# Kernel tuning notes

Measured on AMD Instinct MI355X. Metric: run time of the kernel, lower is better.

Reference implementation:

```python
import jax, jax.numpy as jnp
import numpy as np
import math

DIM = 1024
NUM_HEADS = 16
HEAD_DIM = DIM // NUM_HEADS
EPS = 1e-6
DILATED = 2
WINDOW = 2  # window_size init arg; actual window = L * WINDOW per side


def setup_inputs() -> dict:
    key = jax.random.key(0)
    ks = jax.random.split(key, 14)
    B, S = 1, 8704
    x = jax.random.normal(ks[0], (B, S, DIM), jnp.float32)
    ang = jax.random.uniform(ks[1], (S, HEAD_DIM // 2), jnp.float32, -jnp.pi, jnp.pi)
    freqs_cos = jnp.cos(ang)
    freqs_sin = jnp.sin(ang)
    def lin(k):
        return 0.02 * jax.random.normal(k, (DIM, DIM), jnp.float32)
    def bias(k):
        return 0.01 * jax.random.normal(k, (DIM,), jnp.float32)
    return {
        'x': x, 'freqs_cos': freqs_cos, 'freqs_sin': freqs_sin,
        'wq': lin(ks[2]), 'bq': bias(ks[3]),
        'wk': lin(ks[4]), 'bk': bias(ks[5]),
        'wv': lin(ks[6]), 'bv': bias(ks[7]),
        'wo': lin(ks[8]), 'bo': bias(ks[9]),
        'gq': 1.0 + 0.02 * jax.random.normal(ks[10], (DIM,), jnp.float32),
        'gk': 1.0 + 0.02 * jax.random.normal(ks[11], (DIM,), jnp.float32),
        'f': 34, 'L': 256,
    }


def rmsnorm(h, g):
    return h * jax.lax.rsqrt(jnp.mean(h * h, axis=-1, keepdims=True) + EPS) * g


def rope(h, cos, sin):
    # h: [B,S,D] viewed as interleaved complex pairs per head, rotated by unit freqs
    B, S, D = h.shape
    hp = h.reshape(B, S, NUM_HEADS, HEAD_DIM // 2, 2)
    a, b = hp[..., 0], hp[..., 1]
    c = cos[None, :, None, :]
    s = sin[None, :, None, :]
    ra = a * c - b * s
    rb = a * s + b * c
    return jnp.stack([ra, rb], axis=-1).reshape(B, S, D)


def windowed_attention(q, k, v, w):
    # sliding-window attention: query i attends keys j with |i-j| <= w (inclusive)
    B, S, D = q.shape
    H, hd = NUM_HEADS, HEAD_DIM
    def heads(t):
        return t.reshape(B, S, H, hd).transpose(0, 2, 1, 3)  # [B,H,S,hd]
    qh, kh, vh = heads(q), heads(k), heads(v)
    C = w  # block size == window -> only 3 neighbor key blocks per query block
    pad = (-S) % C
    Sp = S + pad
    nb = Sp // C
    def blocks(t):
        return jnp.pad(t, ((0, 0), (0, 0), (0, pad), (0, 0))).reshape(B, H, nb, C, hd)
    qb = blocks(qh)
    def win(t):
        tb = jnp.pad(blocks(t), ((0, 0), (0, 0), (1, 1), (0, 0), (0, 0)))
        return jnp.concatenate([tb[:, :, i:i + nb] for i in range(3)], axis=3)  # [B,H,nb,3C,hd]
    kw_, vw_ = win(kh), win(vh)
    scores = jnp.einsum('bhnqd,bhnkd->bhnqk', qb, kw_) * (1.0 / math.sqrt(hd))
    qi = jnp.arange(nb)[:, None, None] * C + jnp.arange(C)[None, :, None]      # [nb,C,1]
    kj = (jnp.arange(nb)[:, None, None] - 1) * C + jnp.arange(3 * C)[None, None, :]  # [nb,1,3C]
    valid = (kj >= 0) & (kj < S) & (qi - kj <= w) & (kj - qi <= w)
    scores = jnp.where(valid, scores, -1e9)
    p = jax.nn.softmax(scores, axis=-1)
    o = jnp.einsum('bhnqk,bhnkd->bhnqd', p, vw_)
    return o.reshape(B, H, Sp, hd)[:, :, :S].transpose(0, 2, 1, 3).reshape(B, S, D)


def reference(x, freqs_cos, freqs_sin, wq, bq, wk, bk, wv, bv, wo, bo, gq, gk, f, L):
    B, S, D = x.shape
    q = rope(rmsnorm(x @ wq + bq, gq), freqs_cos, freqs_sin)
    k = rope(rmsnorm(x @ wk + bk, gk), freqs_cos, freqs_sin)
    v = x @ wv + bv
    w = L * WINDOW
    use_dilated = DILATED > 1 and S // (DILATED * L) > 1
    if use_dilated:
        blk = DILATED * L
        pad_len = blk - S % blk  # == blk when S % blk == 0 (faithful to torch code)
        Sp = S + pad_len
        n = Sp // blk
        def padd(t):
            return jnp.pad(t, ((0, 0), (0, pad_len), (0, 0)))
        def dil(t):
            # 'b (n d l) c -> (b d) (n l) c'
            return t.reshape(B, n, DILATED, L, D).transpose(0, 2, 1, 3, 4).reshape(B * DILATED, n * L, D)
        q, k, v = dil(padd(q)), dil(padd(k)), dil(padd(v))
    o = windowed_attention(q, k, v, w)
    out = o @ wo + bo
    if use_dilated:
        # '(b d) (n l) c -> b (n d l) c', then drop pad
        out = out.reshape(B, DILATED, n, L, D).transpose(0, 2, 1, 3, 4).reshape(B, n * DILATED * L, D)
        out = out[:, :S]
    return out
```

## Files before the change

### kernel.cpp

```cpp
#include <hip/hip_runtime.h>
#include <hip/hip_bf16.h>
#include <stdint.h>

#define DIM 1024
#define NH 16
#define HD 64
#define S_ORIG 8704
#define WIN 512

typedef __attribute__((ext_vector_type(8))) short short8;
typedef __attribute__((ext_vector_type(4))) float f32x4;
typedef __attribute__((ext_vector_type(16))) float f32x16;

__device__ __forceinline__ float bf2f(unsigned short u) {
    return __uint_as_float(((unsigned int)u) << 16);
}
__device__ __forceinline__ unsigned short f2bf(float f) {
    unsigned int x = __float_as_uint(f);
    unsigned int r = x + 0x7fffu + ((x >> 16) & 1u);
    return (unsigned short)(r >> 16);
}
__device__ __forceinline__ unsigned int cvtpk(float lo, float hi) {
    unsigned int r;
    asm("v_cvt_pk_bf16_f32 %0, %1, %2" : "=v"(r) : "v"(lo), "v"(hi));
    return r;
}
__device__ __forceinline__ float fexp2(float x) {
#if __has_builtin(__builtin_amdgcn_exp2f)
    return __builtin_amdgcn_exp2f(x);
#else
    float r;
    asm("v_exp_f32 %0, %1" : "=v"(r) : "v"(x));
    return r;
#endif
}

#define GLD_LDS(gptr, lptr) \
    __builtin_amdgcn_global_load_lds((const __attribute__((address_space(1))) void*)(gptr), \
                                     (__attribute__((address_space(3))) void*)(lptr), 16, 0, 0)

#define FBAR() do { __asm__ volatile("" ::: "memory"); \
                    __builtin_amdgcn_s_barrier(); \
                    __asm__ volatile("" ::: "memory"); } while (0)

__global__ __launch_bounds__(256) void prep(const float* __restrict__ x,
                                            unsigned short* __restrict__ xb,
                                            const float* __restrict__ w0,
                                            const float* __restrict__ w1,
                                            const float* __restrict__ w2,
                                            const float* __restrict__ w3,
                                            unsigned short* __restrict__ wt) {
    __shared__ float ts[64][65];
    const int bx = blockIdx.x;
    const int t = threadIdx.x;
    if (bx < 8704) {
        int i = (bx * 256 + t) * 4;
        float4 v = *(const float4*)(x + i);
        ushort4 o;
        o.x = f2bf(v.x); o.y = f2bf(v.y); o.z = f2bf(v.z); o.w = f2bf(v.w);
        *(ushort4*)(xb + i) = o;
        return;
    }
    const int b = bx - 8704;
    const int z = b >> 8;
    const int rem = b & 255;
    const int kb = (rem >> 4) * 64, nb = (rem & 15) * 64;
    const float* w = z == 0 ? w0 : z == 1 ? w1 : z == 2 ? w2 : w3;
    unsigned short* o = wt + (size_t)z * DIM * DIM;
    const int c = t & 63, r4 = t >> 6;
#pragma unroll
    for (int rr = 0; rr < 16; rr++) {
        int row = rr * 4 + r4;
        ts[row][c] = w[(size_t)(kb + row) * DIM + nb + c];
    }
    __syncthreads();
#pragma unroll
    for (int rr = 0; rr < 16; rr++) {
        int nl = rr * 4 + r4;
        o[(size_t)(nb + nl) * DIM + kb + c] = f2bf(ts[c][nl]);
    }
}

__device__ __forceinline__ void gemm_step(const unsigned short* __restrict__ pa,
                                          const unsigned short* __restrict__ pb,
                                          int wr, int wc, int r, int jsw,
                                          f32x4 acc[4][4]) {
    short8 af[4], bfr[4];
#pragma unroll
    for (int i = 0; i < 4; i++)
        af[i] = *(const short8*)&pa[(wr * 64 + i * 16 + r) * 32 + jsw];
#pragma unroll
    for (int j = 0; j < 4; j++)
        bfr[j] = *(const short8*)&pb[(wc * 64 + j * 16 + r) * 32 + jsw];
#pragma unroll
    for (int i = 0; i < 4; i++)
#pragma unroll
        for (int j = 0; j < 4; j++)
            acc[i][j] = __builtin_amdgcn_mfma_f32_16x16x32_bf16(af[i], bfr[j], acc[i][j], 0, 0, 0);
}

template <int OUTF32>
__global__ __launch_bounds__(256) void gemm_bf16(const unsigned short* __restrict__ A,
                                                 const unsigned short* __restrict__ Bt,
                                                 const float* __restrict__ b0,
                                                 const float* __restrict__ b1,
                                                 const float* __restrict__ b2,
                                                 void* __restrict__ Cout) {
    __shared__ __align__(16) unsigned short As[3][128 * 32];
    __shared__ __align__(16) unsigned short Bs[3][128 * 32];
    const int z = blockIdx.z;
    const unsigned short* B = Bt + (size_t)z * DIM * DIM;
    const float* bias = z == 0 ? b0 : (z == 1 ? b1 : b2);
    const int m0 = blockIdx.x * 128, n0 = blockIdx.y * 128;
    const int tid = threadIdx.x;
    const int lane = tid & 63, wv = tid >> 6;
    const int wr = wv >> 1, wc = wv & 1;
    const int quad = lane >> 4, r = lane & 15;

    f32x4 acc[4][4];
#pragma unroll
    for (int i = 0; i < 4; i++)
#pragma unroll
        for (int j = 0; j < 4; j++)
#pragma unroll
            for (int t4 = 0; t4 < 4; t4++) acc[i][j][t4] = 0.0f;

    const unsigned short* a_base = A + (size_t)m0 * DIM;
    const unsigned short* b_base = B + (size_t)n0 * DIM;
    const int c0 = wv * 128 + lane;
    const int r0 = c0 >> 2, o0 = (((c0 & 3) ^ ((c0 >> 3) & 3))) * 8;
    const int c1 = c0 + 64;
    const int r1 = c1 >> 2, o1 = (((c1 & 3) ^ ((c1 >> 3) & 3))) * 8;
    const int ld0 = (wv * 128) * 8, ld1 = (wv * 128 + 64) * 8;

    const int jsw = (quad ^ ((r >> 1) & 3)) * 8;

#define ISSUE_STEP(k0_, abuf_, bbuf_) do {                                  \
        GLD_LDS(a_base + (size_t)r0 * DIM + (k0_) + o0, (abuf_) + ld0);     \
        GLD_LDS(a_base + (size_t)r1 * DIM + (k0_) + o1, (abuf_) + ld1);     \
        GLD_LDS(b_base + (size_t)r0 * DIM + (k0_) + o0, (bbuf_) + ld0);     \
        GLD_LDS(b_base + (size_t)r1 * DIM + (k0_) + o1, (bbuf_) + ld1);     \
    } while (0)

    unsigned short *pa0 = &As[0][0], *pa1 = &As[1][0], *pa2 = &As[2][0];
    unsigned short *pb0 = &Bs[0][0], *pb1 = &Bs[1][0], *pb2 = &Bs[2][0];

    ISSUE_STEP(0, pa0, pb0);
    ISSUE_STEP(32, pa1, pb1);

#pragma unroll 3
    for (int k0 = 0; k0 < DIM - 64; k0 += 32) {
        FBAR();
        ISSUE_STEP(k0 + 64, pa2, pb2);
        __asm__ volatile("s_waitcnt vmcnt(8)" ::: "memory");
        __builtin_amdgcn_sched_barrier(0);
        FBAR();
        gemm_step(pa0, pb0, wr, wc, r, jsw, acc);
        unsigned short* t;
        t = pa0; pa0 = pa1; pa1 = pa2; pa2 = t;
        t = pb0; pb0 = pb1; pb1 = pb2; pb2 = t;
    }
    __asm__ volatile("s_waitcnt vmcnt(4)" ::: "memory");
    __builtin_amdgcn_sched_barrier(0);
    FBAR();
    gemm_step(pa0, pb0, wr, wc, r, jsw, acc);
    {
        unsigned short* t;
        t = pa0; pa0 = pa1; pa1 = pa2; pa2 = t;
        t = pb0; pb0 = pb1; pb1 = pb2; pb2 = t;
    }
    __asm__ volatile("s_waitcnt vmcnt(0)" ::: "memory");
    __builtin_amdgcn_sched_barrier(0);
    FBAR();
    gemm_step(pa0, pb0, wr, wc, r, jsw, acc);
#undef ISSUE_STEP

#pragma unroll
    for (int i = 0; i < 4; i++) {
        const int row = m0 + wr * 64 + i * 16 + quad * 4;
#pragma unroll
        for (int j = 0; j < 4; j++) {
            const int col = n0 + wc * 64 + j * 16 + r;
            const float bvl = bias[col];
#pragma unroll
            for (int t4 = 0; t4 < 4; t4++) {
                float vv = acc[i][j][t4] + bvl;
                if (OUTF32) {
                    ((float*)Cout)[(size_t)(row + t4) * DIM + col] = vv;
                } else {
                    ((unsigned short*)Cout)[(size_t)z * S_ORIG * DIM + (size_t)(row + t4) * DIM + col] = f2bf(vv);
                }
            }
        }
    }
}

__global__ __launch_bounds__(256) void norm_rope(unsigned short* __restrict__ hq,
                                                 unsigned short* __restrict__ hk,
                                                 const float* __restrict__ gq,
                                                 const float* __restrict__ gk,
                                                 const float* __restrict__ fcos,
                                                 const float* __restrict__ fsin) {
    const int z = blockIdx.y;
    unsigned short* h = z == 0 ? hq : hk;
    const float* g = z == 0 ? gq : gk;
    const int w = threadIdx.x >> 6, lane = threadIdx.x & 63;
    const int srow = blockIdx.x * 4 + w;
    unsigned short* hp = h + (size_t)srow * DIM;
    const int p0 = lane * 8, p1 = 512 + lane * 8;

    union { int4 i4; unsigned short u[8]; } r0, r1, o0, o1;
    r0.i4 = *(const int4*)(hp + p0);
    r1.i4 = *(const int4*)(hp + p1);
    float v[16];
#pragma unroll
    for (int j = 0; j < 8; j++) { v[j] = bf2f(r0.u[j]); v[8 + j] = bf2f(r1.u[j]); }

    float ss = 0.0f;
#pragma unroll
    for (int j = 0; j < 16; j++) ss += v[j] * v[j];
#pragma unroll
    for (int off = 1; off < 64; off <<= 1) ss += __shfl_xor(ss, off, 64);
    const float rinv = rsqrtf(ss * (1.0f / DIM) + 1e-6f);

    float4 ga = *(const float4*)(g + p0), gb = *(const float4*)(g + p0 + 4);
    float4 gc = *(const float4*)(g + p1), gd = *(const float4*)(g + p1 + 4);
    const float* gg[4] = {&ga.x, &gb.x, &gc.x, &gd.x};
#pragma unroll
    for (int q4 = 0; q4 < 4; q4++)
#pragma unroll
        for (int j = 0; j < 4; j++) v[q4 * 4 + j] *= rinv * gg[q4][j];

    const int i0 = (p0 & 63) >> 1;
    float4 cs = *(const float4*)(fcos + (size_t)srow * 32 + i0);
    float4 sn = *(const float4*)(fsin + (size_t)srow * 32 + i0);
    const float* cp = &cs.x;
    const float* sp = &sn.x;
#pragma unroll
    for (int seg = 0; seg < 2; seg++) {
        unsigned short* uo = seg == 0 ? o0.u : o1.u;
#pragma unroll
        for (int pr = 0; pr < 4; pr++) {
            const float a = v[seg * 8 + pr * 2], b = v[seg * 8 + pr * 2 + 1];
            uo[pr * 2]     = f2bf(a * cp[pr] - b * sp[pr]);
            uo[pr * 2 + 1] = f2bf(a * sp[pr] + b * cp[pr]);
        }
    }
    *(int4*)(hp + p0) = o0.i4;
    *(int4*)(hp + p1) = o1.i4;
}

__device__ __forceinline__ void softmax16(f32x16& s, int kk0, int hi4, int qi,
                                          bool edge, float& lsum) {
#pragma unroll
    for (int reg = 0; reg < 16; reg++) {
        float e = fexp2(s[reg]);
        if (edge) {
            const int kj = kk0 + (reg & 3) + 8 * (reg >> 2) + hi4;
            const int dl = qi - kj;
            if (dl > WIN || dl < -WIN) e = 0.0f;
        }
        s[reg] = e;
        lsum += e;
    }
}

__device__ __forceinline__ short8 mkfrag(const f32x16& p, int base) {
    unsigned int a0 = cvtpk(p[base + 0], p[base + 1]);
    unsigned int b0 = cvtpk(p[base + 4], p[base + 5]);
    unsigned int a1 = cvtpk(p[base + 2], p[base + 3]);
    unsigned int b1 = cvtpk(p[base + 6], p[base + 7]);
    asm volatile("v_permlane32_swap_b32 %0, %1" : "+v"(a0), "+v"(b0));
    asm volatile("v_permlane32_swap_b32 %0, %1" : "+v"(a1), "+v"(b1));
    union { unsigned int w[4]; short8 s; } u;
    u.w[0] = a0; u.w[1] = a1; u.w[2] = b0; u.w[3] = b1;
    return u.s;
}

__device__ __forceinline__ void pack_write_v(unsigned short* __restrict__ Vt,
                                             int4 a0i, int4 a1i, int vt_d0, int vkc, int vko) {
    union { int4 i4; unsigned int w[4]; } a0, a1;
    a0.i4 = a0i; a1.i4 = a1i;
#pragma unroll
    for (int dw = 0; dw < 4; dw++) {
        unsigned int lo = __builtin_amdgcn_perm(a1.w[dw], a0.w[dw], 0x05040100u);
        unsigned int hw = __builtin_amdgcn_perm(a1.w[dw], a0.w[dw], 0x07060302u);
        *(unsigned int*)&Vt[(vt_d0 + dw * 2) * 64 + ((vkc ^ (dw * 2)) << 3) + vko] = lo;
        *(unsigned int*)&Vt[(vt_d0 + dw * 2 + 1) * 64 + ((vkc ^ (dw * 2 + 1)) << 3) + vko] = hw;
    }
}

__global__ __launch_bounds__(256) void attn(const unsigned short* __restrict__ qkv,
                                            unsigned short* __restrict__ ob) {
    __shared__ __align__(16) unsigned short Ks[2][64 * 64];
    __shared__ __align__(16) unsigned short Vt[64 * 64];

    const int head = blockIdx.x >> 1;
    const int d = blockIdx.x & 1;
    const int t0 = blockIdx.y * 2, t1 = t0 + 1;
    const int tid = threadIdx.x;
    const int lane = tid & 63, wv = tid >> 6;
    const int hi = lane >> 5, q32 = lane & 31;
    const int sw8 = (q32 & 7);

    const unsigned short* qb = qkv;
    const unsigned short* kb = qkv + (size_t)S_ORIG * DIM;
    const unsigned short* vb = qkv + (size_t)2 * S_ORIG * DIM;

    const int tw = t0 + (wv >> 1);
    const int qi = tw * 64 + (wv & 1) * 32 + q32;
    const int og_q = ((qi >> 8) << 9) + d * 256 + (qi & 255);

    short8 qf[4];
    {
        const float QSC = 0.125f * 1.44269504088896f;
        const unsigned short* qrow = qb + (size_t)og_q * DIM + head * HD + hi * 8;
#pragma unroll
        for (int kd = 0; kd < 4; kd++) {
            union { int4 i4; unsigned short u[8]; short8 s8; } iv, ov;
            iv.i4 = *(const int4*)(qrow + kd * 16);
#pragma unroll
            for (int j = 0; j < 8; j++) ov.u[j] = f2bf(bf2f(iv.u[j]) * QSC);
            qf[kd] = ov.s8;
        }
    }

    f32x16 o0, o1;
#pragma unroll
    for (int i = 0; i < 16; i++) { o0[i] = 0.0f; o1[i] = 0.0f; }
    float lsum = 0.0f;

    const int kt_lo = (t0 - 8 > 0) ? (t0 - 8) : 0;
    const int kt_hi = (t1 + 8 < 67) ? (t1 + 8) : 67;

    const int krow0 = tid >> 3;
    const int kgc = ((tid & 7) ^ (krow0 & 7)) * 8;

    const int vt_kk = (tid & 31) * 2, vt_d0 = (tid >> 5) * 8;
    const int vkc = vt_kk >> 3, vko = vt_kk & 7;

#define ISSUE_K(kbase_, bufb_) do {                                              \
        const int kj0_ = (kbase_) + krow0;                                       \
        const int ok0_ = ((kj0_ >> 8) << 9) + d * 256 + (kj0_ & 255);            \
        GLD_LDS(kb + (size_t)ok0_ * DIM + head * HD + kgc, (bufb_) + wv * 512);  \
        const int kj1_ = kj0_ + 32;                                              \
        const int ok1_ = ((kj1_ >> 8) << 9) + d * 256 + (kj1_ & 255);            \
        GLD_LDS(kb + (size_t)ok1_ * DIM + head * HD + kgc, (bufb_) + 2048 + wv * 512); \
    } while (0)

#define LOAD_V(kbase_, a0_, a1_) do {                                            \
        const int kj_ = (kbase_) + vt_kk;                                        \
        const int ok_ = ((kj_ >> 8) << 9) + d * 256 + (kj_ & 255);               \
        (a0_) = *(const int4*)(vb + (size_t)ok_ * DIM + head * HD + vt_d0);      \
        (a1_) = *(const int4*)(vb + (size_t)(ok_ + 1) * DIM + head * HD + vt_d0);\
    } while (0)

    ISSUE_K(kt_lo * 64, &Ks[0][0]);
    int4 vc0, vc1;
    LOAD_V(kt_lo * 64, vc0, vc1);

    int cur = 0;
    for (int kt = kt_lo; kt <= kt_hi; kt++) {
        const int kbase = kt * 64;
        FBAR();

        const int knb = ((kt < kt_hi) ? (kt + 1) : kt_hi) * 64;
        ISSUE_K(knb, &Ks[cur ^ 1][0]);
        int4 vn0, vn1;
        LOAD_V(knb, vn0, vn1);

        __asm__ volatile("s_waitcnt vmcnt(4)" ::: "memory");
        __builtin_amdgcn_sched_barrier(0);

        pack_write_v(&Vt[0], vc0, vc1, vt_d0, vkc, vko);
        __asm__ volatile("s_waitcnt lgkmcnt(0)" ::: "memory");
        FBAR();

        if (kt >= tw - 8 && kt <= tw + 8) {
            const bool edge = (kt == tw - 8) || (kt == tw + 8);
            const unsigned short* K = &Ks[cur][0];

            f32x16 s0, s1;
#pragma unroll
            for (int i = 0; i < 16; i++) { s0[i] = 0.0f; s1[i] = 0.0f; }
#pragma unroll
            for (int kd = 0; kd < 4; kd++) {
                const int c = ((kd * 2 + hi) ^ sw8) << 3;
                short8 k0 = *(const short8*)&K[q32 * 64 + c];
                short8 k1 = *(const short8*)&K[(32 + q32) * 64 + c];
                s0 = __builtin_amdgcn_mfma_f32_32x32x16_bf16(k0, qf[kd], s0, 0, 0, 0);
                s1 = __builtin_amdgcn_mfma_f32_32x32x16_bf16(k1, qf[kd], s1, 0, 0, 0);
            }

            const int hi4 = hi * 4;
            softmax16(s0, kbase, hi4, qi, edge, lsum);
            softmax16(s1, kbase + 32, hi4, qi, edge, lsum);
            short8 pf0 = mkfrag(s0, 0), pf1 = mkfrag(s0, 8);
            short8 pf2 = mkfrag(s1, 0), pf3 = mkfrag(s1, 8);

#pragma unroll
            for (int kw = 0; kw < 4; kw++) {
                const int c = ((kw * 2 + hi) ^ sw8) << 3;
                short8 v0 = *(const short8*)&Vt[q32 * 64 + c];
                short8 v1 = *(const short8*)&Vt[(32 + q32) * 64 + c];
                const short8 pf = kw == 0 ? pf0 : kw == 1 ? pf1 : kw == 2 ? pf2 : pf3;
                o0 = __builtin_amdgcn_mfma_f32_32x32x16_bf16(v0, pf, o0, 0, 0, 0);
                o1 = __builtin_amdgcn_mfma_f32_32x32x16_bf16(v1, pf, o1, 0, 0, 0);
            }
        }

        vc0 = vn0; vc1 = vn1;
        cur ^= 1;
    }
#undef ISSUE_K
#undef LOAD_V

    __asm__ volatile("" :: "v"(vc0.x), "v"(vc0.y), "v"(vc0.z), "v"(vc0.w),
                          "v"(vc1.x), "v"(vc1.y), "v"(vc1.z), "v"(vc1.w));
    __asm__ volatile("s_waitcnt vmcnt(0)" ::: "memory");

    lsum += __shfl_xor(lsum, 32, 64);
    {
        const int cnt = (qi + WIN < 4607 ? qi + WIN : 4607) - 4351;
        if (cnt > 0) lsum += (float)cnt;
    }
    const float linv = 1.0f / lsum;

    unsigned short* obase = ob + (size_t)og_q * DIM + head * HD + hi * 4;
#pragma unroll
    for (int g = 0; g < 4; g++) {
        ushort4 u0, u1;
        u0.x = f2bf(o0[g * 4 + 0] * linv);
        u0.y = f2bf(o0[g * 4 + 1] * linv);
        u0.z = f2bf(o0[g * 4 + 2] * linv);
        u0.w = f2bf(o0[g * 4 + 3] * linv);
        *(ushort4*)(obase + g * 8) = u0;
        u1.x = f2bf(o1[g * 4 + 0] * linv);
        u1.y = f2bf(o1[g * 4 + 1] * linv);
        u1.z = f2bf(o1[g * 4 + 2] * linv);
        u1.w = f2bf(o1[g * 4 + 3] * linv);
        *(ushort4*)(obase + 32 + g * 8) = u1;
    }
}

extern "C" void kernel_launch(void* const* d_in, const int* in_sizes, int n_in,
                              void* d_out, int out_size, void* d_ws, size_t ws_size,
                              hipStream_t stream) {
    const float* x    = (const float*)d_in[0];
    const float* fcos = (const float*)d_in[1];
    const float* fsin = (const float*)d_in[2];
    const float* wq   = (const float*)d_in[3];
    const float* bq   = (const float*)d_in[4];
    const float* wk   = (const float*)d_in[5];
    const float* bk   = (const float*)d_in[6];
    const float* wv   = (const float*)d_in[7];
    const float* bv   = (const float*)d_in[8];
    const float* wo   = (const float*)d_in[9];
    const float* bo   = (const float*)d_in[10];
    const float* gq   = (const float*)d_in[11];
    const float* gk   = (const float*)d_in[12];

    char* ws = (char*)d_ws;
    unsigned short* xb = (unsigned short*)(ws);
    unsigned short* wt = (unsigned short*)(ws + 17825792);
    unsigned short* h  = (unsigned short*)(ws + 26214400);
    unsigned short* ob = (unsigned short*)(ws + 79691776);
    float* outp = (float*)d_out;

    prep<<<9728, 256, 0, stream>>>(x, xb, wq, wk, wv, wo, wt);
    gemm_bf16<0><<<dim3(68, 8, 3), 256, 0, stream>>>(xb, wt, bq, bk, bv, (void*)h);
    norm_rope<<<dim3(2176, 2), 256, 0, stream>>>(h, h + (size_t)S_ORIG * DIM, gq, gk, fcos, fsin);
    attn<<<dim3(32, 34), 256, 0, stream>>>(h, ob);
    gemm_bf16<1><<<dim3(68, 8, 1), 256, 0, stream>>>(ob, wt + (size_t)3 * DIM * DIM, bo, bo, bo, (void*)outp);
}
```

Baseline: 305.4 us.

## Enlarge GEMM tiles to 256x256 with 8 waves and 64-wide K double buffering

Rewrites the bf16 GEMM to use 256x256 output tiles with 512 threads (8 waves, each computing 128x64), K-steps of 64, and a double-buffered LDS pipeline with an XOR swizzle over 8 chunks. It also raises wave priority around the MFMA bursts. The aim is more arithmetic per LDS and global byte and fewer barriers per unit of work. In exchange the grid shrinks sharply: 408 blocks for QKV and only 136 for the output projection, which underfills the 256 CUs. LDS per block also grows to 128KB.

```diff
diff --git a/kernel.cpp b/kernel.cpp
--- a/kernel.cpp
+++ b/kernel.cpp
@@ -81,45 +81,69 @@
     }
 }
 
-__device__ __forceinline__ void gemm_step(const unsigned short* __restrict__ pa,
-                                          const unsigned short* __restrict__ pb,
-                                          int wr, int wc, int r, int jsw,
-                                          f32x4 acc[4][4]) {
-    short8 af[4], bfr[4];
-#pragma unroll
-    for (int i = 0; i < 4; i++)
-        af[i] = *(const short8*)&pa[(wr * 64 + i * 16 + r) * 32 + jsw];
-#pragma unroll
-    for (int j = 0; j < 4; j++)
-        bfr[j] = *(const short8*)&pb[(wc * 64 + j * 16 + r) * 32 + jsw];
-#pragma unroll
-    for (int i = 0; i < 4; i++)
-#pragma unroll
-        for (int j = 0; j < 4; j++)
-            acc[i][j] = __builtin_amdgcn_mfma_f32_16x16x32_bf16(af[i], bfr[j], acc[i][j], 0, 0, 0);
+__device__ __forceinline__ void issue_tile(const unsigned short* __restrict__ a_base,
+                                           const unsigned short* __restrict__ b_base,
+                                           int kt, unsigned short* ab, unsigned short* bb,
+                                           int krow, int kgc, int wv) {
+    const int kk = kt * 64;
+#pragma unroll
+    for (int g = 0; g < 4; g++) {
+        GLD_LDS(a_base + (size_t)(g * 64 + krow) * DIM + kk + kgc, ab + g * 4096 + wv * 512);
+        GLD_LDS(b_base + (size_t)(g * 64 + krow) * DIM + kk + kgc, bb + g * 4096 + wv * 512);
+    }
+}
+
+__device__ __forceinline__ void compute_tile(const unsigned short* __restrict__ ab,
+                                             const unsigned short* __restrict__ bb,
+                                             int wm, int wn, int quad, int r16,
+                                             f32x4 acc[8][4]) {
+    const int sw = r16 & 7;
+#pragma unroll
+    for (int ks = 0; ks < 2; ks++) {
+        const int ch = ((ks * 4 + quad) ^ sw) * 8;
+        short8 bfr[4];
+#pragma unroll
+        for (int nf = 0; nf < 4; nf++)
+            bfr[nf] = *(const short8*)&bb[(wn * 64 + nf * 16 + r16) * 64 + ch];
+#pragma unroll
+        for (int mh = 0; mh < 2; mh++) {
+            short8 af[4];
+#pragma unroll
+            for (int m4 = 0; m4 < 4; m4++)
+                af[m4] = *(const short8*)&ab[(wm * 128 + mh * 64 + m4 * 16 + r16) * 64 + ch];
+            __builtin_amdgcn_s_setprio(1);
+#pragma unroll
+            for (int m4 = 0; m4 < 4; m4++)
+#pragma unroll
+                for (int nf = 0; nf < 4; nf++)
+                    acc[mh * 4 + m4][nf] = __builtin_amdgcn_mfma_f32_16x16x32_bf16(
+                        af[m4], bfr[nf], acc[mh * 4 + m4][nf], 0, 0, 0);
+            __builtin_amdgcn_s_setprio(0);
+        }
+    }
 }
 
 template <int OUTF32>
-__global__ __launch_bounds__(256) void gemm_bf16(const unsigned short* __restrict__ A,
+__global__ __launch_bounds__(512) void gemm_bf16(const unsigned short* __restrict__ A,
                                                  const unsigned short* __restrict__ Bt,
                                                  const float* __restrict__ b0,
                                                  const float* __restrict__ b1,
                                                  const float* __restrict__ b2,
                                                  void* __restrict__ Cout) {
-    __shared__ __align__(16) unsigned short As[3][128 * 32];
-    __shared__ __align__(16) unsigned short Bs[3][128 * 32];
+    __shared__ __align__(16) unsigned short Ab[2][256 * 64];
+    __shared__ __align__(16) unsigned short Bb[2][256 * 64];
     const int z = blockIdx.z;
     const unsigned short* B = Bt + (size_t)z * DIM * DIM;
     const float* bias = z == 0 ? b0 : (z == 1 ? b1 : b2);
-    const int m0 = blockIdx.x * 128, n0 = blockIdx.y * 128;
+    const int m0 = blockIdx.x * 256, n0 = blockIdx.y * 256;
     const int tid = threadIdx.x;
     const int lane = tid & 63, wv = tid >> 6;
-    const int wr = wv >> 1, wc = wv & 1;
-    const int quad = lane >> 4, r = lane & 15;
-
-    f32x4 acc[4][4];
-#pragma unroll
-    for (int i = 0; i < 4; i++)
+    const int wm = wv >> 2, wn = wv & 3;
+    const int quad = lane >> 4, r16 = lane & 15;
+
+    f32x4 acc[8][4];
+#pragma unroll
+    for (int i = 0; i < 8; i++)
 #pragma unroll
         for (int j = 0; j < 4; j++)
 #pragma unroll
@@ -127,64 +151,41 @@
 
     const unsigned short* a_base = A + (size_t)m0 * DIM;
     const unsigned short* b_base = B + (size_t)n0 * DIM;
-    const int c0 = wv * 128 + lane;
-    const int r0 = c0 >> 2, o0 = (((c0 & 3) ^ ((c0 >> 3) & 3))) * 8;
-    const int c1 = c0 + 64;
-    const int r1 = c1 >> 2, o1 = (((c1 & 3) ^ ((c1 >> 3) & 3))) * 8;
-    const int ld0 = (wv * 128) * 8, ld1 = (wv * 128 + 64) * 8;
-
-    const int jsw = (quad ^ ((r >> 1) & 3)) * 8;
-
-#define ISSUE_STEP(k0_, abuf_, bbuf_) do {                                  \
-        GLD_LDS(a_base + (size_t)r0 * DIM + (k0_) + o0, (abuf_) + ld0);     \
-        GLD_LDS(a_base + (size_t)r1 * DIM + (k0_) + o1, (abuf_) + ld1);     \
-        GLD_LDS(b_base + (size_t)r0 * DIM + (k0_) + o0, (bbuf_) + ld0);     \
-        GLD_LDS(b_base + (size_t)r1 * DIM + (k0_) + o1, (bbuf_) + ld1);     \
+
+    const int krow = tid >> 3;
+    const int kgc = ((tid & 7) ^ (krow & 7)) * 8;
+
+    issue_tile(a_base, b_base, 0, &Ab[0][0], &Bb[0][0], krow, kgc, wv);
+    issue_tile(a_base, b_base, 1, &Ab[1][0], &Bb[1][0], krow, kgc, wv);
+
+#define GBODY(kt_, buf_, WAITI, DOISSUE) do {                                   \
+        __asm__ volatile(WAITI ::: "memory");                                   \
+        __builtin_amdgcn_sched_barrier(0);                                      \
+        FBAR();           \
+        compute_tile(&Ab[buf_][0], &Bb[buf_][0], wm, wn, quad, r16, acc);       \
+        FBAR();               \
+        if (DOISSUE) issue_tile(a_base, b_base, (kt_) + 2,                      \
+                                &Ab[buf_][0], &Bb[buf_][0], krow, kgc, wv);     \
     } while (0)
 
-    unsigned short *pa0 = &As[0][0], *pa1 = &As[1][0], *pa2 = &As[2][0];
-    unsigned short *pb0 = &Bs[0][0], *pb1 = &Bs[1][0], *pb2 = &Bs[2][0];
-
-    ISSUE_STEP(0, pa0, pb0);
-    ISSUE_STEP(32, pa1, pb1);
-
-#pragma unroll 3
-    for (int k0 = 0; k0 < DIM - 64; k0 += 32) {
-        FBAR();
-        ISSUE_STEP(k0 + 64, pa2, pb2);
-        __asm__ volatile("s_waitcnt vmcnt(8)" ::: "memory");
-        __builtin_amdgcn_sched_barrier(0);
-        FBAR();
-        gemm_step(pa0, pb0, wr, wc, r, jsw, acc);
-        unsigned short* t;
-        t = pa0; pa0 = pa1; pa1 = pa2; pa2 = t;
-        t = pb0; pb0 = pb1; pb1 = pb2; pb2 = t;
-    }
-    __asm__ volatile("s_waitcnt vmcnt(4)" ::: "memory");
-    __builtin_amdgcn_sched_barrier(0);
-    FBAR();
-    gemm_step(pa0, pb0, wr, wc, r, jsw, acc);
-    {
-        unsigned short* t;
-        t = pa0; pa0 = pa1; pa1 = pa2; pa2 = t;
-        t = pb0; pb0 = pb1; pb1 = pb2; pb2 = t;
-    }
-    __asm__ volatile("s_waitcnt vmcnt(0)" ::: "memory");
-    __builtin_amdgcn_sched_barrier(0);
-    FBAR();
-    gemm_step(pa0, pb0, wr, wc, r, jsw, acc);
-#undef ISSUE_STEP
-
-#pragma unroll
-    for (int i = 0; i < 4; i++) {
-        const int row = m0 + wr * 64 + i * 16 + quad * 4;
-#pragma unroll
-        for (int j = 0; j < 4; j++) {
-            const int col = n0 + wc * 64 + j * 16 + r;
+    for (int t = 0; t < 14; t += 2) {
+        GBODY(t,     0, "s_waitcnt vmcnt(8)", 1);
+        GBODY(t + 1, 1, "s_waitcnt vmcnt(8)", 1);
+    }
+    GBODY(14, 0, "s_waitcnt vmcnt(8)", 0);
+    GBODY(15, 1, "s_waitcnt vmcnt(0)", 0);
+#undef GBODY
+
+#pragma unroll
+    for (int mf = 0; mf < 8; mf++) {
+        const int row = m0 + wm * 128 + mf * 16 + quad * 4;
+#pragma unroll
+        for (int nf = 0; nf < 4; nf++) {
+            const int col = n0 + wn * 64 + nf * 16 + r16;
             const float bvl = bias[col];
 #pragma unroll
             for (int t4 = 0; t4 < 4; t4++) {
-                float vv = acc[i][j][t4] + bvl;
+                float vv = acc[mf][nf][t4] + bvl;
                 if (OUTF32) {
                     ((float*)Cout)[(size_t)(row + t4) * DIM + col] = vv;
                 } else {
@@ -468,8 +469,8 @@
     float* outp = (float*)d_out;
 
     prep<<<9728, 256, 0, stream>>>(x, xb, wq, wk, wv, wo, wt);
-    gemm_bf16<0><<<dim3(68, 8, 3), 256, 0, stream>>>(xb, wt, bq, bk, bv, (void*)h);
+    gemm_bf16<0><<<dim3(34, 4, 3), 512, 0, stream>>>(xb, wt, bq, bk, bv, (void*)h);
     norm_rope<<<dim3(2176, 2), 256, 0, stream>>>(h, h + (size_t)S_ORIG * DIM, gq, gk, fcos, fsin);
     attn<<<dim3(32, 34), 256, 0, stream>>>(h, ob);
-    gemm_bf16<1><<<dim3(68, 8, 1), 256, 0, stream>>>(ob, wt + (size_t)3 * DIM * DIM, bo, bo, bo, (void*)outp);
-}
+    gemm_bf16<1><<<dim3(34, 4, 1), 512, 0, stream>>>(ob, wt + (size_t)3 * DIM * DIM, bo, bo, bo, (void*)outp);
+}
```

Measured after the change: 311.5 us. +2.0%, slower.

## Triple-buffer K and double-buffer V tiles to drop one barrier per iteration

Applied to the files above, without the earlier changes.

Moves the attention K-tile prefetch from double to triple buffering, with a two-tile lookahead, and double-buffers the transposed V tile. This lets the V transpose write for the next tile overlap the current tile's MFMA compute and removes the second workgroup barrier inside the loop. The cost is more LDS per block (about 40KB instead of 24KB), which may lower occupancy, plus an extra prologue stage.

```diff
diff --git a/kernel.cpp b/kernel.cpp
--- a/kernel.cpp
+++ b/kernel.cpp
@@ -292,8 +292,8 @@
 
 __global__ __launch_bounds__(256) void attn(const unsigned short* __restrict__ qkv,
                                             unsigned short* __restrict__ ob) {
-    __shared__ __align__(16) unsigned short Ks[2][64 * 64];
-    __shared__ __align__(16) unsigned short Vt[64 * 64];
+    __shared__ __align__(16) unsigned short Ks[3][64 * 64];
+    __shared__ __align__(16) unsigned short Vt2[2][64 * 64];
 
     const int head = blockIdx.x >> 1;
     const int d = blockIdx.x & 1;
@@ -339,8 +339,8 @@
     const int vt_kk = (tid & 31) * 2, vt_d0 = (tid >> 5) * 8;
     const int vkc = vt_kk >> 3, vko = vt_kk & 7;
 
-#define ISSUE_K(kbase_, bufb_) do {                                              \
-        const int kj0_ = (kbase_) + krow0;                                       \
+#define ISSUE_K(kt_, bufb_) do {                                                 \
+        const int kj0_ = (kt_) * 64 + krow0;                                     \
         const int ok0_ = ((kj0_ >> 8) << 9) + d * 256 + (kj0_ & 255);            \
         GLD_LDS(kb + (size_t)ok0_ * DIM + head * HD + kgc, (bufb_) + wv * 512);  \
         const int kj1_ = kj0_ + 32;                                              \
@@ -348,37 +348,47 @@
         GLD_LDS(kb + (size_t)ok1_ * DIM + head * HD + kgc, (bufb_) + 2048 + wv * 512); \
     } while (0)
 
-#define LOAD_V(kbase_, a0_, a1_) do {                                            \
-        const int kj_ = (kbase_) + vt_kk;                                        \
+#define LOAD_V(kt_, a0_, a1_) do {                                               \
+        const int kj_ = (kt_) * 64 + vt_kk;                                      \
         const int ok_ = ((kj_ >> 8) << 9) + d * 256 + (kj_ & 255);               \
         (a0_) = *(const int4*)(vb + (size_t)ok_ * DIM + head * HD + vt_d0);      \
         (a1_) = *(const int4*)(vb + (size_t)(ok_ + 1) * DIM + head * HD + vt_d0);\
     } while (0)
 
-    ISSUE_K(kt_lo * 64, &Ks[0][0]);
+    unsigned short *k0p = &Ks[0][0], *k1p = &Ks[1][0], *k2p = &Ks[2][0];
+    unsigned short *vtr = &Vt2[0][0], *vtw = &Vt2[1][0];
     int4 vc0, vc1;
-    LOAD_V(kt_lo * 64, vc0, vc1);
-
-    int cur = 0;
+
+    {
+        ISSUE_K(kt_lo, k0p);
+        int4 vA0, vA1;
+        LOAD_V(kt_lo, vA0, vA1);
+        const int ktp1 = (kt_lo + 1 <= kt_hi) ? kt_lo + 1 : kt_hi;
+        ISSUE_K(ktp1, k1p);
+        LOAD_V(ktp1, vc0, vc1);
+        __asm__ volatile("s_waitcnt vmcnt(4)" ::: "memory");
+        __builtin_amdgcn_sched_barrier(0);
+        pack_write_v(vtr, vA0, vA1, vt_d0, vkc, vko);
+        __asm__ volatile("s_waitcnt lgkmcnt(0)" ::: "memory");
+    }
+
     for (int kt = kt_lo; kt <= kt_hi; kt++) {
-        const int kbase = kt * 64;
         FBAR();
 
-        const int knb = ((kt < kt_hi) ? (kt + 1) : kt_hi) * 64;
-        ISSUE_K(knb, &Ks[cur ^ 1][0]);
+        const int knb = (kt + 2 <= kt_hi) ? kt + 2 : kt_hi;
+        ISSUE_K(knb, k2p);
         int4 vn0, vn1;
         LOAD_V(knb, vn0, vn1);
 
         __asm__ volatile("s_waitcnt vmcnt(4)" ::: "memory");
         __builtin_amdgcn_sched_barrier(0);
 
-        pack_write_v(&Vt[0], vc0, vc1, vt_d0, vkc, vko);
-        __asm__ volatile("s_waitcnt lgkmcnt(0)" ::: "memory");
-        FBAR();
+        pack_write_v(vtw, vc0, vc1, vt_d0, vkc, vko);
 
         if (kt >= tw - 8 && kt <= tw + 8) {
             const bool edge = (kt == tw - 8) || (kt == tw + 8);
-            const unsigned short* K = &Ks[cur][0];
+            const unsigned short* K = k0p;
+            const int kbase = kt * 64;
 
             f32x16 s0, s1;
 #pragma unroll
@@ -401,16 +411,19 @@
 #pragma unroll
             for (int kw = 0; kw < 4; kw++) {
                 const int c = ((kw * 2 + hi) ^ sw8) << 3;
-                short8 v0 = *(const short8*)&Vt[q32 * 64 + c];
-                short8 v1 = *(const short8*)&Vt[(32 + q32) * 64 + c];
+                short8 v0 = *(const short8*)&vtr[q32 * 64 + c];
+                short8 v1 = *(const short8*)&vtr[(32 + q32) * 64 + c];
                 const short8 pf = kw == 0 ? pf0 : kw == 1 ? pf1 : kw == 2 ? pf2 : pf3;
                 o0 = __builtin_amdgcn_mfma_f32_32x32x16_bf16(v0, pf, o0, 0, 0, 0);
                 o1 = __builtin_amdgcn_mfma_f32_32x32x16_bf16(v1, pf, o1, 0, 0, 0);
             }
         }
 
+        __asm__ volatile("s_waitcnt lgkmcnt(0)" ::: "memory");
+
+        unsigned short* tp = k0p; k0p = k1p; k1p = k2p; k2p = tp;
+        tp = vtr; vtr = vtw; vtw = tp;
         vc0 = vn0; vc1 = vn1;
-        cur ^= 1;
     }
 #undef ISSUE_K
 #undef LOAD_V
```

Result: no change. 310.4 us (+1.6%).
